# Optimization experiments

Measured on AMD Instinct MI355X. Metric: run time of the kernel, lower is better.

## Reference

```python
import jax, jax.numpy as jnp
import numpy as np

B, N, T, D, M, HOPS = 32, 300, 12, 64, 16, 2

def setup_inputs() -> dict:
    key = jax.random.key(0)
    ks = jax.random.split(key, 12)
    inp = {
        "X": jax.random.normal(ks[0], (B, D, N, T), dtype=jnp.float32),
        "timeEmbedding": jax.random.normal(ks[1], (B, N, T, D), dtype=jnp.float32),
        "adjW": jax.random.normal(ks[2], (N, D), dtype=jnp.float32) * (1.0 / np.sqrt(D)),
        "adjB": jnp.zeros((N,), dtype=jnp.float32),
        "trainW1": jax.random.normal(ks[3], (N, M), dtype=jnp.float32) * 0.1,
        "trainW2": jax.random.normal(ks[4], (M, D * D), dtype=jnp.float32) * 0.1,
        "alpha1": jax.random.normal(ks[5], (N, M), dtype=jnp.float32) * 0.1,
        "alpha2": jax.random.normal(ks[6], (M, N), dtype=jnp.float32) * 0.1,
        "beta1": jax.random.normal(ks[7], (N, M), dtype=jnp.float32) * 0.1,
        "beta2": jax.random.normal(ks[8], (M, N), dtype=jnp.float32) * 0.1,
        "gcnW": jax.random.normal(ks[9], (D, D * (HOPS + 1)), dtype=jnp.float32) * (1.0 / np.sqrt(D * (HOPS + 1))),
        "gcnB": jnp.zeros((D,), dtype=jnp.float32),
    }
    return inp

def reference(X, timeEmbedding, adjW, adjB, trainW1, trainW2, alpha1, alpha2, beta1, beta2, gcnW, gcnB):
    # timeEmbedding: [B,N,T,D] -> [B,T,N,D]
    te = jnp.transpose(timeEmbedding, (0, 2, 1, 3))
    # learned adjacency: A[b,t,n,k]
    A = jnp.sin(jnp.einsum('btnd,kd->btnk', te, adjW) + adjB)  # Linear(dmodel->N)
    A = (alpha1 @ alpha2) * A            # elementwise scale by [N,N], broadcast over b,t
    A = jax.nn.relu(A + beta1 @ beta2)
    # X: [B,D,N,T] -> [B,T,N,D]
    Xp = jnp.transpose(X, (0, 3, 2, 1))
    # per-node weight matrices [N,D,D]
    W = (trainW1 @ trainW2).reshape(N, D, D)
    Hs = [Xp]
    Hb = Xp
    for _ in range(HOPS):
        Hnow = jnp.einsum('btnk,btkd->btnd', A, Hb)      # adjacency aggregation
        Hnow = jnp.einsum('btnk,nkd->btnd', Hnow, W)     # per-node distinct matmul
        pre = Xp + Hnow
        Hnow = jax.nn.sigmoid(pre) * jnp.tanh(pre)        # gated residual
        Hs.append(Hnow)
        Hb = Hnow
    H = jnp.concatenate(Hs, axis=3)                       # [B,T,N,D*(hops+1)]
    Hout = jnp.einsum('btnf,df->btnd', H, gcnW) + gcnB    # gcnLinear (dropout = identity in eval)
    return jnp.transpose(Hout, (0, 3, 2, 1))              # [B,D,N,T]
```

## Files before the change

kernel.cpp:

```cpp
#include <hip/hip_runtime.h>

#define Nq 300
#define Tq 12
#define Dq 64
#define Mq 16
#define BTq 384
#define DDq (Dq*Dq)
#define Fq (Dq*3)
#define NP 320

typedef short bf8_t __attribute__((ext_vector_type(8)));
typedef float f4_t  __attribute__((ext_vector_type(4)));

__device__ __forceinline__ unsigned short f2bf(float f) {
    unsigned u = __float_as_uint(f);
    u = (u + 0x7FFFu + ((u >> 16) & 1u)) >> 16;
    return (unsigned short)u;
}
__device__ __forceinline__ float bf2f(unsigned short u) {
    return __uint_as_float((unsigned)u << 16);
}
__device__ __forceinline__ unsigned cvtpk(float lo, float hi) {
    unsigned r;
    asm("v_cvt_pk_bf16_f32 %0, %1, %2" : "=v"(r) : "v"(lo), "v"(hi));
    return r;
}
__device__ __forceinline__ float4 ld4(const float* p) { return *(const float4*)p; }

__device__ __forceinline__ bf8_t pack8(float4 a, float4 b) {
    union { unsigned u[4]; bf8_t v; } q;
    q.u[0] = cvtpk(a.x, a.y); q.u[1] = cvtpk(a.z, a.w);
    q.u[2] = cvtpk(b.x, b.y); q.u[3] = cvtpk(b.z, b.w);
    return q.v;
}

__device__ __forceinline__ float gatef(float p) {
    float pc = fminf(fmaxf(p, -30.f), 30.f);
    float u = __expf(pc);
    return u * (u - 1.f) / (u * u + 1.f);
}

__global__ void __launch_bounds__(256) kprep_all(
    const float* __restrict__ a1, const float* __restrict__ a2,
    const float* __restrict__ b1, const float* __restrict__ b2,
    const float* __restrict__ w1, const float* __restrict__ w2,
    const float* __restrict__ adjW, const float* __restrict__ adjB,
    const float* __restrict__ X,
    unsigned* __restrict__ ABt, unsigned short* __restrict__ Wt,
    unsigned short* __restrict__ adjWb, float* __restrict__ adjBp,
    unsigned short* __restrict__ Xp_t, unsigned short* __restrict__ Xp_nb)
{
    __shared__ char smem[64 * 308 * 2];
    const int vb = blockIdx.x;
    const int tid = threadIdx.x;

    if (vb < 400) {
        const int tile = vb;
        const int reg = tid & 3, lane = tid >> 2;
        const int nt = tile % 5;  int r1 = tile / 5;
        const int w  = r1 % 4;    int r2 = r1 / 4;
        const int c  = r2 % 5;    const int qi = r2 / 5;
        const int n = qi*80 + nt*16 + (lane & 15);
        const int k = c*64 + w*16 + (lane >> 4)*4 + reg;
        unsigned outv = 0u;
        if (n < Nq && k < Nq) {
            float sa = 0.f, sb = 0.f;
            #pragma unroll
            for (int m = 0; m < Mq; ++m) {
                sa = fmaf(a1[n*Mq+m], a2[m*Nq+k], sa);
                sb = fmaf(b1[n*Mq+m], b2[m*Nq+k], sb);
            }
            outv = cvtpk(sa, sb);
        }
        ABt[tile*256 + tid] = outv;
    } else if (vb < 700) {
        float* sT = (float*)smem;
        __shared__ float sw1[Mq];
        const int n = vb - 400;
        if (tid < Mq) sw1[tid] = w1[n*Mq + tid];
        __syncthreads();
        for (int i = tid; i < DDq; i += 256) {
            int k = i >> 6, d = i & 63;
            float s = 0.f;
            #pragma unroll
            for (int m = 0; m < Mq; ++m) s = fmaf(sw1[m], w2[m*DDq + i], s);
            sT[d*65 + k] = s;
        }
        __syncthreads();
        for (int i = tid; i < DDq; i += 256) {
            int d = i >> 6, k = i & 63;
            Wt[(size_t)n*DDq + i] = f2bf(sT[d*65 + k]);
        }
    } else if (vb < 780) {
        int e = (vb - 700) * 256 + tid;
        if (e < NP * 64) {
            int k = e >> 6, d = e & 63;
            adjWb[e] = (k < Nq) ? f2bf(adjW[k*Dq + d]) : (unsigned short)0;
        }
        if (e < NP) adjBp[e] = (e < Nq) ? adjB[e] : 0.f;
    } else {
        unsigned short* sT = (unsigned short*)smem;
        const int bx = vb - 780;
        const int b = bx / 24, sub = bx % 24;
        const int tile = sub >> 1, half = sub & 1;
        const int n0 = tile * 25, d0 = half * 32;
        for (int i = tid; i < 32 * 75; i += 256) {
            int dl = i / 75, jq = i - dl*75, j = jq*4;
            float4 v = ld4(&X[(size_t)(b*64 + d0 + dl)*3600 + n0*12 + j]);
            *(uint2*)&sT[dl*308 + j] = make_uint2(cvtpk(v.x, v.y), cvtpk(v.z, v.w));
        }
        __syncthreads();
        for (int wi = tid; wi < 12 * 32 * 25; wi += 256) {
            int nl = wi % 25, rem = wi / 25;
            int dl = rem & 31, t = rem >> 5;
            Xp_t[((size_t)(b*Tq + t)*64 + d0 + dl)*NP + n0 + nl] = sT[dl*308 + nl*12 + t];
        }
        if (tile == 11) {
            for (int wi = tid; wi < 12 * 32 * 20; wi += 256) {
                int e = wi % 20, rem = wi / 20;
                int dl = rem & 31, t = rem >> 5;
                Xp_t[((size_t)(b*Tq + t)*64 + d0 + dl)*NP + 300 + e] = 0;
            }
        }
        for (int wi = tid; wi < 25 * 12 * 8; wi += 256) {
            int dg = wi & 7, rem = wi >> 3;
            int t = rem % 12, nl = rem / 12;
            ushort4 o;
            o.x = sT[(dg*4+0)*308 + nl*12 + t];
            o.y = sT[(dg*4+1)*308 + nl*12 + t];
            o.z = sT[(dg*4+2)*308 + nl*12 + t];
            o.w = sT[(dg*4+3)*308 + nl*12 + t];
            *(ushort4*)&Xp_nb[((size_t)(n0+nl)*BTq + b*Tq + t)*64 + d0 + dg*4] = o;
        }
    }
}

__global__ void __launch_bounds__(256) ktr2(const unsigned short* __restrict__ Hnb,
                                            unsigned short* __restrict__ Ht) {
    __shared__ unsigned short sT[64 * 308];
    const int bt = blockIdx.x;
    const int tid = threadIdx.x;
    for (int i = tid; i < 300 * 16; i += 256) {
        int nl = i >> 4, dg = i & 15;
        ushort4 v = *(const ushort4*)&Hnb[((size_t)nl*BTq + bt)*64 + dg*4];
        sT[(dg*4+0)*308 + nl] = v.x;
        sT[(dg*4+1)*308 + nl] = v.y;
        sT[(dg*4+2)*308 + nl] = v.z;
        sT[(dg*4+3)*308 + nl] = v.w;
    }
    __syncthreads();
    for (int wi = tid; wi < 64 * 80; wi += 256) {
        int kq = wi % 80, d = wi / 80;
        ushort4 o;
        int k = kq * 4;
        o.x = (k+0 < Nq) ? sT[d*308 + k+0] : (unsigned short)0;
        o.y = (k+1 < Nq) ? sT[d*308 + k+1] : (unsigned short)0;
        o.z = (k+2 < Nq) ? sT[d*308 + k+2] : (unsigned short)0;
        o.w = (k+3 < Nq) ? sT[d*308 + k+3] : (unsigned short)0;
        *(ushort4*)&Ht[((size_t)bt*64 + d)*NP + k] = o;
    }
}

template<int HOP>
__global__ void __launch_bounds__(256) kfuse_t(
    const float* __restrict__ te,
    unsigned short* __restrict__ teP,
    const unsigned short* __restrict__ adjWb,
    const float* __restrict__ adjBp,
    const unsigned* __restrict__ ABt,
    const unsigned short* __restrict__ Hb_t,
    unsigned short* __restrict__ Hout_nb)
{
    __shared__ unsigned short sPl[2][80 * 72];
    const int bt = blockIdx.x >> 2, qi = blockIdx.x & 3;
    const int b = bt / Tq, t = bt - b * Tq;
    const int nbase = qi * 80;
    const int tid = threadIdx.x;
    const int w = tid >> 6, lane = tid & 63, quad = lane >> 4, l16 = lane & 15;
    const int dcol = w*16 + l16;

    bf8_t tb0[5], tb1[5];
    #pragma unroll
    for (int nt = 0; nt < 5; ++nt) {
        int n = nbase + nt*16 + l16; if (n > Nq-1) n = Nq-1;
        if (HOP == 1) {
            const float* ter = te + (((size_t)b*Nq + n)*Tq + t)*Dq;
            tb0[nt] = pack8(ld4(ter + quad*8),      ld4(ter + quad*8 + 4));
            tb1[nt] = pack8(ld4(ter + 32 + quad*8), ld4(ter + 36 + quad*8));
            if (w == 0) {
                *(bf8_t*)&teP[((size_t)bt*Nq + n)*64 + quad*8] = tb0[nt];
                *(bf8_t*)&teP[((size_t)bt*Nq + n)*64 + 32 + quad*8] = tb1[nt];
            }
        } else {
            const unsigned short* tr = teP + ((size_t)bt*Nq + n)*64;
            tb0[nt] = *(const bf8_t*)(tr + quad*8);
            tb1[nt] = *(const bf8_t*)(tr + 32 + quad*8);
        }
    }
    f4_t accO[5];
    #pragma unroll
    for (int rt = 0; rt < 5; ++rt) accO[rt] = (f4_t){0.f, 0.f, 0.f, 0.f};

    const unsigned short* hr = Hb_t + ((size_t)bt*64 + dcol)*NP;
    bf8_t hv0 = *(const bf8_t*)(hr + quad*8);
    bf8_t hv1 = *(const bf8_t*)(hr + 32 + quad*8);

    for (int c = 0; c < 5; ++c) {
        const int cbase = c * 64;
        bf8_t nhv0, nhv1;
        if (c < 4) {
            nhv0 = *(const bf8_t*)(hr + cbase + 64 + quad*8);
            nhv1 = *(const bf8_t*)(hr + cbase + 96 + quad*8);
        }
        const unsigned* abbase = ABt + ((((size_t)qi*5 + c)*4 + w)*5)*256 + lane*4;
        uint4 abv[5];
        #pragma unroll
        for (int nt = 0; nt < 5; ++nt) abv[nt] = *(const uint4*)(abbase + nt*256);
        const unsigned short* ar = adjWb + (cbase + w*16 + l16)*64;
        bf8_t ka0 = *(const bf8_t*)(ar + quad*8);
        bf8_t ka1 = *(const bf8_t*)(ar + 32 + quad*8);
        float4 bias4 = ld4(adjBp + cbase + w*16 + quad*4);
        unsigned short* sp = sPl[c & 1];
        #pragma unroll
        for (int nt = 0; nt < 5; ++nt) {
            f4_t p = {0.f, 0.f, 0.f, 0.f};
            p = __builtin_amdgcn_mfma_f32_16x16x32_bf16(ka0, tb0[nt], p, 0, 0, 0);
            p = __builtin_amdgcn_mfma_f32_16x16x32_bf16(ka1, tb1[nt], p, 0, 0, 0);
            uint4 ab = abv[nt];
            float s0 = fmaxf(fmaf(__uint_as_float(ab.x << 16), __sinf(p[0] + bias4.x),
                                  __uint_as_float(ab.x & 0xFFFF0000u)), 0.f);
            float s1 = fmaxf(fmaf(__uint_as_float(ab.y << 16), __sinf(p[1] + bias4.y),
                                  __uint_as_float(ab.y & 0xFFFF0000u)), 0.f);
            float s2 = fmaxf(fmaf(__uint_as_float(ab.z << 16), __sinf(p[2] + bias4.z),
                                  __uint_as_float(ab.z & 0xFFFF0000u)), 0.f);
            float s3 = fmaxf(fmaf(__uint_as_float(ab.w << 16), __sinf(p[3] + bias4.w),
                                  __uint_as_float(ab.w & 0xFFFF0000u)), 0.f);
            *(uint2*)&sp[(nt*16 + l16)*72 + w*16 + quad*4] =
                make_uint2(cvtpk(s0, s1), cvtpk(s2, s3));
        }
        __syncthreads();
        #pragma unroll
        for (int rt = 0; rt < 5; ++rt) {
            bf8_t p0 = *(const bf8_t*)&sp[(rt*16 + l16)*72 + quad*8];
            bf8_t p1 = *(const bf8_t*)&sp[(rt*16 + l16)*72 + 32 + quad*8];
            accO[rt] = __builtin_amdgcn_mfma_f32_16x16x32_bf16(hv0, p0, accO[rt], 0, 0, 0);
            accO[rt] = __builtin_amdgcn_mfma_f32_16x16x32_bf16(hv1, p1, accO[rt], 0, 0, 0);
        }
        if (c < 4) { hv0 = nhv0; hv1 = nhv1; }
    }
    #pragma unroll
    for (int rt = 0; rt < 5; ++rt) {
        int n = nbase + rt*16 + l16;
        if (n < Nq) {
            *(uint2*)&Hout_nb[((size_t)n*BTq + bt)*64 + w*16 + quad*4] =
                make_uint2(cvtpk(accO[rt][0], accO[rt][1]),
                           cvtpk(accO[rt][2], accO[rt][3]));
        }
    }
}

__global__ void __launch_bounds__(256) kmm(
    const unsigned short* __restrict__ Hagg_nb,
    const unsigned short* __restrict__ Xp_nb,
    const unsigned short* __restrict__ Wt,
    unsigned short* __restrict__ Hout_nb)
{
    const int n = blockIdx.x >> 2, qi = blockIdx.x & 3;
    const int bt0 = qi * 96;
    const int tid = threadIdx.x;
    const int w = tid >> 6, lane = tid & 63, quad = lane >> 4, l16 = lane & 15;
    const int dcol = w*16 + l16;
    const unsigned short* wn = Wt + (size_t)n * DDq + dcol*64;
    bf8_t v0 = *(const bf8_t*)(wn + quad*8);
    bf8_t v1 = *(const bf8_t*)(wn + 32 + quad*8);
    bf8_t a0[6], a1[6];
    #pragma unroll
    for (int rt = 0; rt < 6; ++rt) {
        int r = bt0 + rt*16 + l16;
        const unsigned short* row = Hagg_nb + ((size_t)n*BTq + r)*64;
        a0[rt] = *(const bf8_t*)(row + quad*8);
        a1[rt] = *(const bf8_t*)(row + 32 + quad*8);
    }
    f4_t acc[6];
    #pragma unroll
    for (int rt = 0; rt < 6; ++rt) acc[rt] = (f4_t){0.f, 0.f, 0.f, 0.f};
    #pragma unroll
    for (int rt = 0; rt < 6; ++rt) {
        acc[rt] = __builtin_amdgcn_mfma_f32_16x16x32_bf16(v0, a0[rt], acc[rt], 0, 0, 0);
        acc[rt] = __builtin_amdgcn_mfma_f32_16x16x32_bf16(v1, a1[rt], acc[rt], 0, 0, 0);
    }
    __syncthreads();
    ushort4 xp4[6];
    #pragma unroll
    for (int rt = 0; rt < 6; ++rt) {
        int r = bt0 + rt*16 + l16;
        xp4[rt] = *(const ushort4*)&Xp_nb[((size_t)n*BTq + r)*64 + w*16 + quad*4];
    }
    #pragma unroll
    for (int rt = 0; rt < 6; ++rt) {
        int r = bt0 + rt*16 + l16;
        float g0 = gatef(bf2f(xp4[rt].x) + acc[rt][0]);
        float g1 = gatef(bf2f(xp4[rt].y) + acc[rt][1]);
        float g2 = gatef(bf2f(xp4[rt].z) + acc[rt][2]);
        float g3 = gatef(bf2f(xp4[rt].w) + acc[rt][3]);
        *(uint2*)&Hout_nb[((size_t)n*BTq + r)*64 + w*16 + quad*4] =
            make_uint2(cvtpk(g0, g1), cvtpk(g2, g3));
    }
}

__global__ void __launch_bounds__(256) kgcn(
    const unsigned short* __restrict__ Xp_nb, const unsigned short* __restrict__ H1_nb,
    const unsigned short* __restrict__ H2_nb, const float* __restrict__ gcnW,
    const float* __restrict__ gcnB, float* __restrict__ out)
{
    const int bid = blockIdx.x;
    const int b = bid / 57, rem = bid % 57;
    const int tile = rem / 3, rg = rem % 3;
    const int n0 = tile * 16;
    const int rows = (tile == 18) ? 144 : 192;
    const int r0base = rg * 64;
    const int tid = threadIdx.x;
    const int w = tid >> 6, lane = tid & 63, quad = lane >> 4, l16 = lane & 15;
    const int dcol = w*16 + l16;
    const float bias = gcnB[dcol];
    f4_t acc[4];
    #pragma unroll
    for (int rt = 0; rt < 4; ++rt) acc[rt] = (f4_t){0.f, 0.f, 0.f, 0.f};
    const unsigned short* bufs[3] = {Xp_nb, H1_nb, H2_nb};
    #pragma unroll
    for (int c = 0; c < 3; ++c) {
        const unsigned short* buf = bufs[c];
        const float* gwr = gcnW + (size_t)dcol*Fq + c*Dq;
        bf8_t v0 = pack8(ld4(gwr + quad*8),      ld4(gwr + quad*8 + 4));
        bf8_t v1 = pack8(ld4(gwr + 32 + quad*8), ld4(gwr + 36 + quad*8));
        #pragma unroll
        for (int rt = 0; rt < 4; ++rt) {
            int rr = r0base + rt*16;
            if (rr < rows) {
                int r = rr + l16;
                int nl = r / 12, t = r - nl*12;
                int n = n0 + nl; if (n > Nq-1) n = Nq-1;
                const unsigned short* row = buf + ((size_t)n*BTq + b*Tq + t)*64;
                bf8_t a0 = *(const bf8_t*)(row + quad*8);
                bf8_t a1 = *(const bf8_t*)(row + 32 + quad*8);
                acc[rt] = __builtin_amdgcn_mfma_f32_16x16x32_bf16(a0, v0, acc[rt], 0, 0, 0);
                acc[rt] = __builtin_amdgcn_mfma_f32_16x16x32_bf16(a1, v1, acc[rt], 0, 0, 0);
            }
        }
    }
    float* outd = out + (size_t)(b*Dq + dcol)*3600 + n0*12;
    #pragma unroll
    for (int rt = 0; rt < 4; ++rt) {
        int rr = r0base + rt*16;
        if (rr < rows) {
            int r0 = rr + quad*4;
            float4 o = make_float4(acc[rt][0] + bias, acc[rt][1] + bias,
                                   acc[rt][2] + bias, acc[rt][3] + bias);
            *(float4*)&outd[r0] = o;
        }
    }
}

extern "C" void kernel_launch(void* const* d_in, const int* in_sizes, int n_in,
                              void* d_out, int out_size, void* d_ws, size_t ws_size,
                              hipStream_t stream) {
    (void)in_sizes; (void)n_in; (void)out_size; (void)ws_size;
    const float* X    = (const float*)d_in[0];
    const float* te   = (const float*)d_in[1];
    const float* adjW = (const float*)d_in[2];
    const float* adjB = (const float*)d_in[3];
    const float* w1   = (const float*)d_in[4];
    const float* w2   = (const float*)d_in[5];
    const float* a1   = (const float*)d_in[6];
    const float* a2   = (const float*)d_in[7];
    const float* b1   = (const float*)d_in[8];
    const float* b2   = (const float*)d_in[9];
    const float* gW   = (const float*)d_in[10];
    const float* gB   = (const float*)d_in[11];
    float* out = (float*)d_out;

    char* ws = (char*)d_ws;
    unsigned*       ABt    = (unsigned*)      (ws);
    unsigned short* adjWb  = (unsigned short*)(ws + 409600);
    float*          adjBp  = (float*)         (ws + 450560);
    unsigned short* Wt     = (unsigned short*)(ws + 451840);
    unsigned short* Xp_t   = (unsigned short*)(ws + 2909440);
    unsigned short* Xp_nb  = (unsigned short*)(ws + 18638080);
    unsigned short* Hagg   = (unsigned short*)(ws + 33383680);
    unsigned short* H1_nb  = (unsigned short*)(ws + 48129280);
    unsigned short* H1_t   = (unsigned short*)(ws + 62874880);
    unsigned short* teP    = (unsigned short*)(ws + 78603520);

    hipLaunchKernelGGL(kprep_all, dim3(1548), dim3(256), 0, stream,
                       a1, a2, b1, b2, w1, w2, adjW, adjB, X,
                       ABt, Wt, adjWb, adjBp, Xp_t, Xp_nb);
    hipLaunchKernelGGL(HIP_KERNEL_NAME(kfuse_t<1>), dim3(1536), dim3(256), 0, stream,
                       te, teP, adjWb, adjBp, ABt, Xp_t, Hagg);
    hipLaunchKernelGGL(kmm,   dim3(1200), dim3(256), 0, stream, Hagg, Xp_nb, Wt, H1_nb);
    hipLaunchKernelGGL(ktr2,  dim3(384),  dim3(256), 0, stream, H1_nb, H1_t);
    hipLaunchKernelGGL(HIP_KERNEL_NAME(kfuse_t<2>), dim3(1536), dim3(256), 0, stream,
                       te, teP, adjWb, adjBp, ABt, H1_t, Hagg);
    hipLaunchKernelGGL(kmm,   dim3(1200), dim3(256), 0, stream, Hagg, Xp_nb, Wt, Hagg);
    hipLaunchKernelGGL(kgcn,  dim3(1824), dim3(256), 0, stream, Xp_nb, H1_nb, Hagg, gW, gB, out);
}
```

Baseline: 289.7 us.

## Stage time-embedding and output through LDS for coalesced accesses in fused kernel

```diff
diff --git a/kernel.cpp b/kernel.cpp
--- a/kernel.cpp
+++ b/kernel.cpp
@@ -140,13 +140,12 @@
     __shared__ unsigned short sT[64 * 308];
     const int bt = blockIdx.x;
     const int tid = threadIdx.x;
-    for (int i = tid; i < 300 * 16; i += 256) {
-        int nl = i >> 4, dg = i & 15;
-        ushort4 v = *(const ushort4*)&Hnb[((size_t)nl*BTq + bt)*64 + dg*4];
-        sT[(dg*4+0)*308 + nl] = v.x;
-        sT[(dg*4+1)*308 + nl] = v.y;
-        sT[(dg*4+2)*308 + nl] = v.z;
-        sT[(dg*4+3)*308 + nl] = v.w;
+    for (int i = tid; i < 300 * 8; i += 256) {
+        int nl = i >> 3, dg = i & 7;
+        bf8_t v = *(const bf8_t*)&Hnb[((size_t)nl*BTq + bt)*64 + dg*8];
+        #pragma unroll
+        for (int k = 0; k < 8; ++k)
+            sT[(dg*8+k)*308 + nl] = (unsigned short)v[k];
     }
     __syncthreads();
     for (int wi = tid; wi < 64 * 80; wi += 256) {
@@ -171,47 +170,57 @@
     const unsigned short* __restrict__ Hb_t,
     unsigned short* __restrict__ Hout_nb)
 {
-    __shared__ unsigned short sPl[2][80 * 72];
+    __shared__ unsigned short sP[80 * 72];
+    __shared__ unsigned short sT[80 * 68];
     const int bt = blockIdx.x >> 2, qi = blockIdx.x & 3;
     const int b = bt / Tq, t = bt - b * Tq;
     const int nbase = qi * 80;
     const int tid = threadIdx.x;
     const int w = tid >> 6, lane = tid & 63, quad = lane >> 4, l16 = lane & 15;
     const int dcol = w*16 + l16;
-
+    const int nrows = (Nq - nbase < 80) ? (Nq - nbase) : 80;
+
+    if (HOP == 1) {
+        #pragma unroll
+        for (int r = 0; r < 5; ++r) {
+            int row = r*16 + (tid >> 4);
+            int col = (tid & 15) * 4;
+            int n = nbase + row; if (n > Nq-1) n = Nq-1;
+            float4 v = ld4(te + (((size_t)b*Nq + n)*Tq + t)*Dq + col);
+            *(uint2*)&sT[row*68 + col] = make_uint2(cvtpk(v.x, v.y), cvtpk(v.z, v.w));
+        }
+    } else {
+        for (int idx = tid; idx < 80*8; idx += 256) {
+            int row = idx >> 3, cg = idx & 7;
+            int n = nbase + row; if (n > Nq-1) n = Nq-1;
+            *(bf8_t*)&sT[row*68 + cg*8] =
+                *(const bf8_t*)&teP[((size_t)bt*Nq + n)*64 + cg*8];
+        }
+    }
+    __syncthreads();
+    if (HOP == 1) {
+        for (int idx = tid; idx < nrows*8; idx += 256) {
+            int row = idx >> 3, cg = idx & 7;
+            *(bf8_t*)&teP[((size_t)bt*Nq + nbase + row)*64 + cg*8] =
+                *(const bf8_t*)&sT[row*68 + cg*8];
+        }
+    }
     bf8_t tb0[5], tb1[5];
     #pragma unroll
     for (int nt = 0; nt < 5; ++nt) {
-        int n = nbase + nt*16 + l16; if (n > Nq-1) n = Nq-1;
-        if (HOP == 1) {
-            const float* ter = te + (((size_t)b*Nq + n)*Tq + t)*Dq;
-            tb0[nt] = pack8(ld4(ter + quad*8),      ld4(ter + quad*8 + 4));
-            tb1[nt] = pack8(ld4(ter + 32 + quad*8), ld4(ter + 36 + quad*8));
-            if (w == 0) {
-                *(bf8_t*)&teP[((size_t)bt*Nq + n)*64 + quad*8] = tb0[nt];
-                *(bf8_t*)&teP[((size_t)bt*Nq + n)*64 + 32 + quad*8] = tb1[nt];
-            }
-        } else {
-            const unsigned short* tr = teP + ((size_t)bt*Nq + n)*64;
-            tb0[nt] = *(const bf8_t*)(tr + quad*8);
-            tb1[nt] = *(const bf8_t*)(tr + 32 + quad*8);
-        }
-    }
+        const unsigned short* tr = &sT[(nt*16 + l16)*68];
+        tb0[nt] = *(const bf8_t*)(tr + quad*8);
+        tb1[nt] = *(const bf8_t*)(tr + 32 + quad*8);
+    }
+
     f4_t accO[5];
     #pragma unroll
     for (int rt = 0; rt < 5; ++rt) accO[rt] = (f4_t){0.f, 0.f, 0.f, 0.f};
 
     const unsigned short* hr = Hb_t + ((size_t)bt*64 + dcol)*NP;
-    bf8_t hv0 = *(const bf8_t*)(hr + quad*8);
-    bf8_t hv1 = *(const bf8_t*)(hr + 32 + quad*8);
 
     for (int c = 0; c < 5; ++c) {
         const int cbase = c * 64;
-        bf8_t nhv0, nhv1;
-        if (c < 4) {
-            nhv0 = *(const bf8_t*)(hr + cbase + 64 + quad*8);
-            nhv1 = *(const bf8_t*)(hr + cbase + 96 + quad*8);
-        }
         const unsigned* abbase = ABt + ((((size_t)qi*5 + c)*4 + w)*5)*256 + lane*4;
         uint4 abv[5];
         #pragma unroll
@@ -220,7 +229,10 @@
         bf8_t ka0 = *(const bf8_t*)(ar + quad*8);
         bf8_t ka1 = *(const bf8_t*)(ar + 32 + quad*8);
         float4 bias4 = ld4(adjBp + cbase + w*16 + quad*4);
-        unsigned short* sp = sPl[c & 1];
+        bf8_t hv0 = *(const bf8_t*)(hr + cbase + quad*8);
+        bf8_t hv1 = *(const bf8_t*)(hr + cbase + 32 + quad*8);
+
+        if (c > 0) __syncthreads();
         #pragma unroll
         for (int nt = 0; nt < 5; ++nt) {
             f4_t p = {0.f, 0.f, 0.f, 0.f};
@@ -235,27 +247,29 @@
                                   __uint_as_float(ab.z & 0xFFFF0000u)), 0.f);
             float s3 = fmaxf(fmaf(__uint_as_float(ab.w << 16), __sinf(p[3] + bias4.w),
                                   __uint_as_float(ab.w & 0xFFFF0000u)), 0.f);
-            *(uint2*)&sp[(nt*16 + l16)*72 + w*16 + quad*4] =
+            *(uint2*)&sP[(nt*16 + l16)*72 + w*16 + quad*4] =
                 make_uint2(cvtpk(s0, s1), cvtpk(s2, s3));
         }
         __syncthreads();
         #pragma unroll
         for (int rt = 0; rt < 5; ++rt) {
-            bf8_t p0 = *(const bf8_t*)&sp[(rt*16 + l16)*72 + quad*8];
-            bf8_t p1 = *(const bf8_t*)&sp[(rt*16 + l16)*72 + 32 + quad*8];
+            bf8_t p0 = *(const bf8_t*)&sP[(rt*16 + l16)*72 + quad*8];
+            bf8_t p1 = *(const bf8_t*)&sP[(rt*16 + l16)*72 + 32 + quad*8];
             accO[rt] = __builtin_amdgcn_mfma_f32_16x16x32_bf16(hv0, p0, accO[rt], 0, 0, 0);
             accO[rt] = __builtin_amdgcn_mfma_f32_16x16x32_bf16(hv1, p1, accO[rt], 0, 0, 0);
         }
-        if (c < 4) { hv0 = nhv0; hv1 = nhv1; }
     }
     #pragma unroll
     for (int rt = 0; rt < 5; ++rt) {
-        int n = nbase + rt*16 + l16;
-        if (n < Nq) {
-            *(uint2*)&Hout_nb[((size_t)n*BTq + bt)*64 + w*16 + quad*4] =
-                make_uint2(cvtpk(accO[rt][0], accO[rt][1]),
-                           cvtpk(accO[rt][2], accO[rt][3]));
-        }
+        *(uint2*)&sT[(rt*16 + l16)*68 + w*16 + quad*4] =
+            make_uint2(cvtpk(accO[rt][0], accO[rt][1]),
+                       cvtpk(accO[rt][2], accO[rt][3]));
+    }
+    __syncthreads();
+    for (int idx = tid; idx < nrows*8; idx += 256) {
+        int row = idx >> 3, cg = idx & 7;
+        *(bf8_t*)&Hout_nb[((size_t)(nbase + row)*BTq + bt)*64 + cg*8] =
+            *(const bf8_t*)&sT[row*68 + cg*8];
     }
 }
 
```

New measurement: 288.9 us. About the same (-0.3%).
